# Optimization experiments

Hardware: AMD Instinct MI355X
Metric: run time of the kernel (lower is better)

The kernel has to match this reference:

```python
import jax, jax.numpy as jnp
import numpy as np

B, S, HID = 2, 2048, 2048
NH, NKV, D = 32, 4, 64
N_REP = NH // NKV
EPS = 1e-6
ROPE_THETA = 10000.0


def _rotate_half(x):
    h = x.shape[-1] // 2
    return jnp.concatenate([-x[..., h:], x[..., :h]], axis=-1)


def _rmsnorm(x, gamma):
    # RMSNorm over last dim (head_dim)
    return x * jax.lax.rsqrt(jnp.mean(x * x, axis=-1, keepdims=True) + EPS) * gamma


def setup_inputs() -> dict:
    key = jax.random.key(0)
    ks = jax.random.split(key, 8)
    hidden_states = jax.random.normal(ks[0], (B, S, HID), dtype=jnp.float32)
    # rotary cos/sin tables, shape [B, S, D]
    pos = jnp.arange(S, dtype=jnp.float32)
    inv_freq = 1.0 / (ROPE_THETA ** (jnp.arange(0, D, 2, dtype=jnp.float32) / D))
    freqs = pos[:, None] * inv_freq[None, :]            # [S, D/2]
    emb = jnp.concatenate([freqs, freqs], axis=-1)      # [S, D]
    cos = jnp.broadcast_to(jnp.cos(emb)[None], (B, S, D))
    sin = jnp.broadcast_to(jnp.sin(emb)[None], (B, S, D))
    sc = 0.02
    Wq = jax.random.normal(ks[1], (NH * D, HID), dtype=jnp.float32) * sc
    Wk = jax.random.normal(ks[2], (NKV * D, HID), dtype=jnp.float32) * sc
    Wv = jax.random.normal(ks[3], (NKV * D, HID), dtype=jnp.float32) * sc
    Wg = jax.random.normal(ks[4], (NH * D, HID), dtype=jnp.float32) * sc
    Wo = jax.random.normal(ks[5], (HID, NH * D), dtype=jnp.float32) * sc
    q_gamma = jnp.ones((D,), dtype=jnp.float32)
    k_gamma = jnp.ones((D,), dtype=jnp.float32)
    return dict(hidden_states=hidden_states, cos=cos, sin=sin,
                Wq=Wq, Wk=Wk, Wv=Wv, Wg=Wg, Wo=Wo,
                q_gamma=q_gamma, k_gamma=k_gamma)


def reference(hidden_states, cos, sin, Wq, Wk, Wv, Wg, Wo, q_gamma, k_gamma):
    b, s, _ = hidden_states.shape
    q = (hidden_states @ Wq.T).reshape(b, s, NH, D)
    k = (hidden_states @ Wk.T).reshape(b, s, NKV, D)
    v = (hidden_states @ Wv.T).reshape(b, s, NKV, D)
    gate = hidden_states @ Wg.T                       # [B, S, NH*D]
    # per-head RMSNorm on q/k
    q = _rmsnorm(q, q_gamma)
    k = _rmsnorm(k, k_gamma)
    # [B, H, S, D]
    q = q.transpose(0, 2, 1, 3)
    k = k.transpose(0, 2, 1, 3)
    v = v.transpose(0, 2, 1, 3)
    # RoPE (unsqueeze_dim=1)
    c = cos[:, None, :, :]
    sn = sin[:, None, :, :]
    q = q * c + _rotate_half(q) * sn
    k = k * c + _rotate_half(k) * sn
    # GQA: repeat kv heads
    kr = jnp.repeat(k, N_REP, axis=1)
    vr = jnp.repeat(v, N_REP, axis=1)
    scaling = D ** -0.5
    scores = jnp.einsum('bhqd,bhkd->bhqk', q, kr) * scaling
    w = jax.nn.softmax(scores.astype(jnp.float32), axis=-1).astype(q.dtype)
    out = jnp.einsum('bhqk,bhkd->bhqd', w, vr)
    out = out.transpose(0, 2, 1, 3).reshape(b, s, NH * D)
    out = out * jax.nn.sigmoid(gate)
    return out @ Wo.T
```

## Files before the change

kernel.cpp:

```cpp
#include <hip/hip_runtime.h>


#define LOG2E 1.44269504088896340736f

typedef __attribute__((ext_vector_type(4))) float f32x4;
typedef __attribute__((ext_vector_type(8))) short bf16x8;

__device__ __forceinline__ float bf2f(unsigned short u) {
  union { unsigned u; float f; } x; x.u = ((unsigned)u) << 16; return x.f;
}
__device__ __forceinline__ unsigned short f2bf(float f) {
  union { float f; unsigned u; } x; x.f = f;
  unsigned r = x.u + 0x7fffu + ((x.u >> 16) & 1u);
  return (unsigned short)(r >> 16);
}

__device__ __forceinline__ void async16(void* lds, const void* g) {
  __builtin_amdgcn_global_load_lds(
      (const __attribute__((address_space(1))) unsigned*)g,
      (__attribute__((address_space(3))) unsigned*)lds, 16, 0, 0);
}
__device__ __forceinline__ void lds_fence() {
  __asm__ volatile("s_waitcnt lgkmcnt(0)" ::: "memory");
}

__global__ __launch_bounds__(256) void cvt_all(
    const float* __restrict__ s0, const float* __restrict__ s1,
    const float* __restrict__ s2, const float* __restrict__ s3,
    const float* __restrict__ s4, const float* __restrict__ s5,
    unsigned short* __restrict__ d0, unsigned short* __restrict__ d1,
    unsigned short* __restrict__ d2, unsigned short* __restrict__ d3,
    unsigned short* __restrict__ d4, unsigned short* __restrict__ d5) {
  long i = (long)blockIdx.x * 256 + threadIdx.x;
  const float* s; unsigned short* d; long off;
  if      (i < 2097152) { s = s0; d = d0; off = 0; }
  else if (i < 3145728) { s = s1; d = d1; off = 2097152; }
  else if (i < 3276800) { s = s2; d = d2; off = 3145728; }
  else if (i < 3407872) { s = s3; d = d3; off = 3276800; }
  else if (i < 4456448) { s = s4; d = d4; off = 3407872; }
  else                  { s = s5; d = d5; off = 4456448; }
  long j = i - off;
  float4 v = reinterpret_cast<const float4*>(s)[j];
  ushort4 u;
  u.x = f2bf(v.x); u.y = f2bf(v.y); u.z = f2bf(v.z); u.w = f2bf(v.w);
  reinterpret_cast<ushort4*>(d)[j] = u;
}

__device__ __forceinline__ void gemm_main(
    const unsigned short* __restrict__ A, const unsigned short* __restrict__ W,
    int m0, int n0, int K, unsigned short* As, unsigned short* Bs,
    f32x4 acc[4][4]) {
  const int tid = threadIdx.x;
  const int w = tid >> 6, l = tid & 63, quad = l >> 4, l16 = l & 15;
  const int wm = (w & 1) * 64, wn = (w >> 1) * 64;

  const f32x4 Z4 = {0.f, 0.f, 0.f, 0.f};
#pragma unroll
  for (int i = 0; i < 4; i++)
#pragma unroll
    for (int j = 0; j < 4; j++) acc[i][j] = Z4;

  const int srow = tid >> 2;
  const int scol = (((tid & 3) ^ ((tid >> 3) & 3))) * 8;
  const unsigned short* gA = A + (size_t)(m0 + srow) * K + scol;
  const unsigned short* gB = W + (size_t)(n0 + srow) * K + scol;
  unsigned short* lA = As + tid * 8;
  unsigned short* lB = Bs + tid * 8;
  const int fsw = (quad ^ ((l16 >> 1) & 3)) * 8;

  for (int kb = 0; kb < K; kb += 32) {
    async16(lA,        gA + kb);
    async16(lA + 2048, gA + (size_t)64 * K + kb);
    async16(lB,        gB + kb);
    async16(lB + 2048, gB + (size_t)64 * K + kb);
    __syncthreads();

    bf16x8 af[4], bf[4];
#pragma unroll
    for (int mt = 0; mt < 4; mt++)
      af[mt] = *(const bf16x8*)&As[(wm + mt * 16 + l16) * 32 + fsw];
#pragma unroll
    for (int nt = 0; nt < 4; nt++)
      bf[nt] = *(const bf16x8*)&Bs[(wn + nt * 16 + l16) * 32 + fsw];
#pragma unroll
    for (int mt = 0; mt < 4; mt++)
#pragma unroll
      for (int nt = 0; nt < 4; nt++)
        acc[mt][nt] = __builtin_amdgcn_mfma_f32_16x16x32_bf16(
            af[mt], bf[nt], acc[mt][nt], 0, 0, 0);
    __syncthreads();
  }
}

__global__ __launch_bounds__(256) void gemm_qkvg(
    const unsigned short* __restrict__ X,
    const unsigned short* __restrict__ Wq, const unsigned short* __restrict__ Wk,
    const unsigned short* __restrict__ Wv, const unsigned short* __restrict__ Wg,
    const float* __restrict__ cosb, const float* __restrict__ sinb,
    const float* __restrict__ qg, const float* __restrict__ kg,
    unsigned short* __restrict__ Qn, unsigned short* __restrict__ Kn,
    unsigned short* __restrict__ Vt, unsigned short* __restrict__ gate) {
  __shared__ __attribute__((aligned(16))) unsigned short As[128 * 32];
  __shared__ __attribute__((aligned(16))) unsigned short Bs[128 * 32];
  const int ny = blockIdx.y;
  const unsigned short* W; int n0, type;
  if (ny < 16)      { W = Wq; n0 = ny * 128;        type = 0; }
  else if (ny < 18) { W = Wk; n0 = (ny - 16) * 128; type = 1; }
  else if (ny < 20) { W = Wv; n0 = (ny - 18) * 128; type = 2; }
  else              { W = Wg; n0 = (ny - 20) * 128; type = 3; }
  const int m0 = blockIdx.x * 128;

  f32x4 acc[4][4];
  gemm_main(X, W, m0, n0, 2048, As, Bs, acc);

  const int tid = threadIdx.x;
  const int w = tid >> 6, l = tid & 63, quad = l >> 4, l16 = l & 15;
  const int wm = (w & 1) * 64, wn = (w >> 1) * 64;

  if (type == 3) {
#pragma unroll
    for (int mt = 0; mt < 4; mt++)
#pragma unroll
      for (int r = 0; r < 4; r++) {
        int row = m0 + wm + mt * 16 + quad * 4 + r;
#pragma unroll
        for (int nt = 0; nt < 4; nt++)
          gate[(size_t)row * 2048 + n0 + wn + nt * 16 + l16] =
              f2bf(acc[mt][nt][r]);
      }
    return;
  }
  if (type == 2) {
#pragma unroll
    for (int mt = 0; mt < 4; mt++)
#pragma unroll
      for (int r = 0; r < 4; r++) {
        int row = m0 + wm + mt * 16 + quad * 4 + r;
        int b = row >> 11, s = row & 2047;
#pragma unroll
        for (int nt = 0; nt < 4; nt++) {
          int col = n0 + wn + nt * 16 + l16;
          int kvh = col >> 6, d = col & 63;
          Vt[((size_t)(b * 4 + kvh) * 64 + d) * 2048 + s] =
              f2bf(acc[mt][nt][r]);
        }
      }
    return;
  }

  const float* gamma = (type == 0) ? qg : kg;
  const float scale  = (type == 0) ? 0.125f : LOG2E;
  const int hb = (n0 + wn) >> 6;
  float gv[4];
#pragma unroll
  for (int nt = 0; nt < 4; nt++) gv[nt] = gamma[nt * 16 + l16];

#pragma unroll
  for (int mt = 0; mt < 4; mt++)
#pragma unroll
    for (int r = 0; r < 4; r++) {
      int row = m0 + wm + mt * 16 + quad * 4 + r;
      float ss = 0.f;
#pragma unroll
      for (int nt = 0; nt < 4; nt++) {
        float v = acc[mt][nt][r]; ss += v * v;
      }
#pragma unroll
      for (int off = 1; off < 16; off <<= 1) ss += __shfl_xor(ss, off);
      float rr = rsqrtf(ss * (1.0f / 64.0f) + 1e-6f);
      float xn[4];
#pragma unroll
      for (int nt = 0; nt < 4; nt++) xn[nt] = acc[mt][nt][r] * rr * gv[nt];
      int b = row >> 11, s = row & 2047;
      unsigned short* dst = (type == 0)
          ? Qn + ((size_t)(b * 32 + hb) * 2048 + s) * 64
          : Kn + ((size_t)(b * 4 + hb) * 2048 + s) * 64;
#pragma unroll
      for (int nt = 0; nt < 4; nt++) {
        int d = nt * 16 + l16;
        float rot = (nt < 2) ? -xn[nt ^ 2] : xn[nt ^ 2];
        float cv = cosb[(size_t)row * 64 + d];
        float sv = sinb[(size_t)row * 64 + d];
        dst[d] = f2bf((xn[nt] * cv + rot * sv) * scale);
      }
    }
}

__global__ __launch_bounds__(256) void gemm_out_k(
    const unsigned short* __restrict__ A, const unsigned short* __restrict__ W,
    float* __restrict__ C) {
  __shared__ __attribute__((aligned(16))) unsigned short As[128 * 32];
  __shared__ __attribute__((aligned(16))) unsigned short Bs[128 * 32];
  const int m0 = blockIdx.x * 128, n0 = blockIdx.y * 128;
  f32x4 acc[4][4];
  gemm_main(A, W, m0, n0, 2048, As, Bs, acc);
  const int tid = threadIdx.x;
  const int w = tid >> 6, l = tid & 63, quad = l >> 4, l16 = l & 15;
  const int wm = (w & 1) * 64, wn = (w >> 1) * 64;
#pragma unroll
  for (int mt = 0; mt < 4; mt++)
#pragma unroll
    for (int nt = 0; nt < 4; nt++) {
      int row = m0 + wm + mt * 16 + quad * 4;
      int col = n0 + wn + nt * 16 + l16;
#pragma unroll
      for (int r = 0; r < 4; r++)
        C[(size_t)(row + r) * 2048 + col] = acc[mt][nt][r];
    }
}

__global__ __launch_bounds__(256, 4) void attn(
    const unsigned short* __restrict__ Qn, const unsigned short* __restrict__ Kn,
    const unsigned short* __restrict__ Vt, const unsigned short* __restrict__ gate,
    unsigned short* __restrict__ act) {
  __shared__ __attribute__((aligned(16))) unsigned short smem[20480];
  unsigned short* Ps = smem + 16384;

  const int tid = threadIdx.x, w = tid >> 6, l = tid & 63;
  const int quad = l >> 4, l16 = l & 15, l7 = l16 & 7;
  const int bh = blockIdx.y, b = bh >> 5, h = bh & 31, kvh = h >> 3;
  const int q0 = blockIdx.x * 128;

  const unsigned short* Qg = Qn + ((size_t)(b * 32 + h) * 2048 + q0) * 64;
  const unsigned short* Kg = Kn + (size_t)(b * 4 + kvh) * 2048 * 64;
  const unsigned short* Vg = Vt + (size_t)(b * 4 + kvh) * 64 * 2048;
  unsigned short* Pw = Ps + w * 1024;

  const int kq_src = ((tid & 7) ^ ((tid >> 3) & 7)) * 8;

#pragma unroll
  for (int i = 0; i < 4; i++)
    async16(smem + i * 2048 + tid * 8,
            Qg + (size_t)(i * 32 + (tid >> 3)) * 64 + kq_src);
  __syncthreads();
  bf16x8 qf[2][2];
#pragma unroll
  for (int mt = 0; mt < 2; mt++)
#pragma unroll
    for (int ks = 0; ks < 2; ks++) {
      int row = w * 32 + mt * 16 + l16;
      qf[mt][ks] = *(const bf16x8*)&smem[row * 64 + ((ks * 4 + quad) ^ l7) * 8];
    }
  __syncthreads();

  const f32x4 Z4 = {0.f, 0.f, 0.f, 0.f};
  f32x4 O[2][4];
  float lp[2][4];
#pragma unroll
  for (int mt = 0; mt < 2; mt++) {
#pragma unroll
    for (int nt = 0; nt < 4; nt++) O[mt][nt] = Z4;
#pragma unroll
    for (int r = 0; r < 4; r++) lp[mt][r] = 0.f;
  }

#pragma unroll
  for (int i = 0; i < 2; i++) {
    async16(smem + i * 2048 + tid * 8,
            Kg + (size_t)(i * 32 + (tid >> 3)) * 64 + kq_src);
    async16(smem + 4096 + i * 2048 + tid * 8,
            Vg + (size_t)(i * 32 + (tid >> 3)) * 2048 + kq_src);
  }

  for (int kt = 0; kt < 32; kt++) {
    __syncthreads();

    if (kt < 31) {
      unsigned short* nb = smem + ((kt + 1) & 1) * 8192;
      const int s1 = (kt + 1) * 64;
#pragma unroll
      for (int i = 0; i < 2; i++) {
        async16(nb + i * 2048 + tid * 8,
                Kg + (size_t)(s1 + i * 32 + (tid >> 3)) * 64 + kq_src);
        async16(nb + 4096 + i * 2048 + tid * 8,
                Vg + (size_t)(i * 32 + (tid >> 3)) * 2048 + s1 + kq_src);
      }
    }

    unsigned short* Ks  = smem + (kt & 1) * 8192;
    unsigned short* Vts = Ks + 4096;

    f32x4 sc[2][4];
#pragma unroll
    for (int mt = 0; mt < 2; mt++)
#pragma unroll
      for (int nt = 0; nt < 4; nt++) sc[mt][nt] = Z4;
#pragma unroll
    for (int nt = 0; nt < 4; nt++) {
      int row = nt * 16 + l16;
      bf16x8 kf0 = *(const bf16x8*)&Ks[row * 64 + (quad ^ l7) * 8];
      bf16x8 kf1 = *(const bf16x8*)&Ks[row * 64 + ((4 + quad) ^ l7) * 8];
#pragma unroll
      for (int mt = 0; mt < 2; mt++) {
        sc[mt][nt] = __builtin_amdgcn_mfma_f32_16x16x32_bf16(qf[mt][0], kf0, sc[mt][nt], 0, 0, 0);
        sc[mt][nt] = __builtin_amdgcn_mfma_f32_16x16x32_bf16(qf[mt][1], kf1, sc[mt][nt], 0, 0, 0);
      }
    }

#pragma unroll
    for (int ks2 = 0; ks2 < 2; ks2++) {
#pragma unroll
      for (int mt = 0; mt < 2; mt++)
#pragma unroll
        for (int ntl = 0; ntl < 2; ntl++) {
          int nt = ks2 * 2 + ntl;
#pragma unroll
          for (int r = 0; r < 4; r++) {
            float p = __builtin_amdgcn_exp2f(sc[mt][nt][r]);
            union { float f; unsigned u; } x; x.f = p;
            union { unsigned u; float f; } t; t.u = x.u & 0xffff0000u;
            lp[mt][r] += t.f;
            int q = mt * 16 + quad * 4 + r;
            int c = ntl * 2 + (l16 >> 3);
            int phys = c ^ ((q >> 1) & 3);
            Pw[q * 32 + phys * 8 + l7] = (unsigned short)(x.u >> 16);
          }
        }
      lds_fence();

      bf16x8 pf[2];
#pragma unroll
      for (int mt = 0; mt < 2; mt++) {
        int q = mt * 16 + l16;
        int phys = quad ^ ((l16 >> 1) & 3);
        pf[mt] = *(const bf16x8*)&Pw[q * 32 + phys * 8];
      }
#pragma unroll
      for (int nt2 = 0; nt2 < 4; nt2++) {
        int d = nt2 * 16 + l16;
        bf16x8 vf = *(const bf16x8*)&Vts[d * 64 + ((ks2 * 4 + quad) ^ l7) * 8];
#pragma unroll
        for (int mt = 0; mt < 2; mt++)
          O[mt][nt2] = __builtin_amdgcn_mfma_f32_16x16x32_bf16(
              pf[mt], vf, O[mt][nt2], 0, 0, 0);
      }
      lds_fence();
    }
  }

#pragma unroll
  for (int mt = 0; mt < 2; mt++)
#pragma unroll
    for (int r = 0; r < 4; r++) {
      float s = lp[mt][r];
#pragma unroll
      for (int off = 1; off < 16; off <<= 1) s += __shfl_xor(s, off);
      lp[mt][r] = s;
    }

#pragma unroll
  for (int mt = 0; mt < 2; mt++) {
    float inv[4];
#pragma unroll
    for (int r = 0; r < 4; r++) inv[r] = 1.0f / lp[mt][r];
#pragma unroll
    for (int nt = 0; nt < 4; nt++)
#pragma unroll
      for (int r = 0; r < 4; r++) {
        int srow = q0 + w * 32 + mt * 16 + quad * 4 + r;
        int col = h * 64 + nt * 16 + l16;
        size_t off = (size_t)(b * 2048 + srow) * 2048 + col;
        float g = bf2f(gate[off]);
        float sig = 1.0f / (1.0f + __builtin_amdgcn_exp2f(-g * LOG2E));
        act[off] = f2bf(O[mt][nt][r] * inv[r] * sig);
      }
  }
}

extern "C" void kernel_launch(void* const* d_in, const int* in_sizes, int n_in,
                              void* d_out, int out_size, void* d_ws, size_t ws_size,
                              hipStream_t stream) {
  const float* hid  = (const float*)d_in[0];
  const float* cosb = (const float*)d_in[1];
  const float* sinb = (const float*)d_in[2];
  const float* Wq   = (const float*)d_in[3];
  const float* Wk   = (const float*)d_in[4];
  const float* Wv   = (const float*)d_in[5];
  const float* Wg   = (const float*)d_in[6];
  const float* Wo   = (const float*)d_in[7];
  const float* qg   = (const float*)d_in[8];
  const float* kg   = (const float*)d_in[9];
  float* out = (float*)d_out;

  char* ws = (char*)d_ws;
  unsigned short* Xb   = (unsigned short*)(ws);
  unsigned short* WqB  = (unsigned short*)(ws + 16777216);
  unsigned short* WkB  = (unsigned short*)(ws + 25165824);
  unsigned short* WvB  = (unsigned short*)(ws + 26214400);
  unsigned short* WgB  = (unsigned short*)(ws + 27262976);
  unsigned short* WoB  = (unsigned short*)(ws + 35651584);
  unsigned short* gate = (unsigned short*)(ws + 44040192);
  unsigned short* Qn   = (unsigned short*)(ws + 60817408);
  unsigned short* Kn   = (unsigned short*)(ws + 77594624);
  unsigned short* Vt   = (unsigned short*)(ws + 79691776);
  unsigned short* act = WqB;

  cvt_all<<<dim3(21504), dim3(256), 0, stream>>>(
      hid, Wq, Wk, Wv, Wg, Wo, Xb, WqB, WkB, WvB, WgB, WoB);

  gemm_qkvg<<<dim3(32, 36), dim3(256), 0, stream>>>(
      Xb, WqB, WkB, WvB, WgB, cosb, sinb, qg, kg, Qn, Kn, Vt, gate);

  attn<<<dim3(16, 64), dim3(256), 0, stream>>>(Qn, Kn, Vt, gate, act);

  gemm_out_k<<<dim3(32, 16), dim3(256), 0, stream>>>(act, WoB, out);
}
```

Measured before the change: 395.9 us.

## Pipeline GEMMs with multi-buffered async LDS loads and 128x256 tiles

Replaces the single-buffered 128x128 GEMM main loop with a 128x256 tile run by 512 threads. A is double-buffered and B triple-buffered in LDS, with async global-to-LDS prefetch of the next K-step overlapping the MFMA work. K-steps grow to 64 with an 8-way XOR swizzle, plus explicit barriers, waitcnt and setprio scheduling. The QKVG and output GEMM grids are halved to match. This aims to hide global-load latency and raise reuse per block, at the cost of 128KB of LDS per block, fewer blocks, and fragile hand-tuned synchronisation.

```diff
diff --git a/kernel.cpp b/kernel.cpp
--- a/kernel.cpp
+++ b/kernel.cpp
@@ -46,13 +46,14 @@
   reinterpret_cast<ushort4*>(d)[j] = u;
 }
 
-__device__ __forceinline__ void gemm_main(
+__device__ __forceinline__ void gemm_main_big(
     const unsigned short* __restrict__ A, const unsigned short* __restrict__ W,
-    int m0, int n0, int K, unsigned short* As, unsigned short* Bs,
-    f32x4 acc[4][4]) {
+    int m0, int n0, unsigned short* lds, f32x4 acc[4][4]) {
   const int tid = threadIdx.x;
   const int w = tid >> 6, l = tid & 63, quad = l >> 4, l16 = l & 15;
+  const int l7 = l16 & 7;
   const int wm = (w & 1) * 64, wn = (w >> 1) * 64;
+  const int rlo = tid >> 3, ch = tid & 7;
 
   const f32x4 Z4 = {0.f, 0.f, 0.f, 0.f};
 #pragma unroll
@@ -60,39 +61,102 @@
 #pragma unroll
     for (int j = 0; j < 4; j++) acc[i][j] = Z4;
 
-  const int srow = tid >> 2;
-  const int scol = (((tid & 3) ^ ((tid >> 3) & 3))) * 8;
-  const unsigned short* gA = A + (size_t)(m0 + srow) * K + scol;
-  const unsigned short* gB = W + (size_t)(n0 + srow) * K + scol;
-  unsigned short* lA = As + tid * 8;
-  unsigned short* lB = Bs + tid * 8;
-  const int fsw = (quad ^ ((l16 >> 1) & 3)) * 8;
-
-  for (int kb = 0; kb < K; kb += 32) {
-    async16(lA,        gA + kb);
-    async16(lA + 2048, gA + (size_t)64 * K + kb);
-    async16(lB,        gB + kb);
-    async16(lB + 2048, gB + (size_t)64 * K + kb);
-    __syncthreads();
-
-    bf16x8 af[4], bf[4];
-#pragma unroll
-    for (int mt = 0; mt < 4; mt++)
-      af[mt] = *(const bf16x8*)&As[(wm + mt * 16 + l16) * 32 + fsw];
+  const unsigned short* gA = A + (size_t)(m0 + rlo) * 2048 + ((ch ^ (rlo & 7)) * 8);
+  const unsigned short* gB = W + (size_t)(n0 + rlo) * 2048 + ((ch ^ (rlo & 7)) * 8);
+
+  int arow[4], brow[4];
+#pragma unroll
+  for (int mt = 0; mt < 4; mt++) arow[mt] = (wm + mt * 16 + l16) * 64;
+#pragma unroll
+  for (int nt = 0; nt < 4; nt++) brow[nt] = (wn + nt * 16 + l16) * 64;
+  const int x0 = (quad ^ l7) * 8;
+  const int x1 = ((4 + quad) ^ l7) * 8;
+
+  unsigned short* const bA = lds;
+  unsigned short* const bB = lds + 16384;
+
+  async16(bA + tid * 8,          gA);
+  async16(bA + 4096 + tid * 8,   gA + 131072);
+  async16(bB + tid * 8,          gB);
+  async16(bB + 4096 + tid * 8,   gB + 131072);
+  async16(bB + 8192 + tid * 8,   gB + 262144);
+  async16(bB + 12288 + tid * 8,  gB + 393216);
+  async16(bB + 16384 + tid * 8,  gB + 64);
+  async16(bB + 20480 + tid * 8,  gB + 131072 + 64);
+  async16(bB + 24576 + tid * 8,  gB + 262144 + 64);
+  async16(bB + 28672 + tid * 8,  gB + 393216 + 64);
+  __asm__ volatile("s_waitcnt vmcnt(4)" ::: "memory");
+  __builtin_amdgcn_s_barrier();
+
+  int cb = 0;
+  for (int t = 0; t < 32; ++t) {
+    unsigned short* cbA = bA + (t & 1) * 8192;
+    unsigned short* cbB = bB + cb * 16384;
+
+    if (t < 31) {
+      unsigned short* nA = bA + ((t + 1) & 1) * 8192;
+      const int ko = (t + 1) * 64;
+      async16(nA + tid * 8,        gA + ko);
+      async16(nA + 4096 + tid * 8, gA + 131072 + ko);
+    }
+    bf16x8 a0[4], b0[4];
+#pragma unroll
+    for (int mt = 0; mt < 4; mt++)
+      a0[mt] = *(const bf16x8*)&cbA[arow[mt] + x0];
 #pragma unroll
     for (int nt = 0; nt < 4; nt++)
-      bf[nt] = *(const bf16x8*)&Bs[(wn + nt * 16 + l16) * 32 + fsw];
+      b0[nt] = *(const bf16x8*)&cbB[brow[nt] + x0];
+    __builtin_amdgcn_s_barrier();
+    __asm__ volatile("s_waitcnt lgkmcnt(0)" ::: "memory");
+    __builtin_amdgcn_sched_barrier(0);
+    __builtin_amdgcn_s_setprio(1);
 #pragma unroll
     for (int mt = 0; mt < 4; mt++)
 #pragma unroll
       for (int nt = 0; nt < 4; nt++)
         acc[mt][nt] = __builtin_amdgcn_mfma_f32_16x16x32_bf16(
-            af[mt], bf[nt], acc[mt][nt], 0, 0, 0);
-    __syncthreads();
-  }
-}
-
-__global__ __launch_bounds__(256) void gemm_qkvg(
+            a0[mt], b0[nt], acc[mt][nt], 0, 0, 0);
+    __builtin_amdgcn_s_setprio(0);
+    __builtin_amdgcn_s_barrier();
+
+    if (t < 30) {
+      int nb = cb + 2; if (nb >= 3) nb -= 3;
+      unsigned short* nB = bB + nb * 16384;
+      const int ko = (t + 2) * 64;
+      async16(nB + tid * 8,         gB + ko);
+      async16(nB + 4096 + tid * 8,  gB + 131072 + ko);
+      async16(nB + 8192 + tid * 8,  gB + 262144 + ko);
+      async16(nB + 12288 + tid * 8, gB + 393216 + ko);
+    }
+    bf16x8 a1[4], b1[4];
+#pragma unroll
+    for (int mt = 0; mt < 4; mt++)
+      a1[mt] = *(const bf16x8*)&cbA[arow[mt] + x1];
+#pragma unroll
+    for (int nt = 0; nt < 4; nt++)
+      b1[nt] = *(const bf16x8*)&cbB[brow[nt] + x1];
+    __builtin_amdgcn_s_barrier();
+    __asm__ volatile("s_waitcnt lgkmcnt(0)" ::: "memory");
+    __builtin_amdgcn_sched_barrier(0);
+    __builtin_amdgcn_s_setprio(1);
+#pragma unroll
+    for (int mt = 0; mt < 4; mt++)
+#pragma unroll
+      for (int nt = 0; nt < 4; nt++)
+        acc[mt][nt] = __builtin_amdgcn_mfma_f32_16x16x32_bf16(
+            a1[mt], b1[nt], acc[mt][nt], 0, 0, 0);
+    __builtin_amdgcn_s_setprio(0);
+    if (t < 30) {
+      __asm__ volatile("s_waitcnt vmcnt(4)" ::: "memory");
+    } else if (t == 30) {
+      __asm__ volatile("s_waitcnt vmcnt(0)" ::: "memory");
+    }
+    __builtin_amdgcn_s_barrier();
+    cb++; if (cb == 3) cb = 0;
+  }
+}
+
+__global__ __launch_bounds__(512, 2) void gemm_qkvg(
     const unsigned short* __restrict__ X,
     const unsigned short* __restrict__ Wq, const unsigned short* __restrict__ Wk,
     const unsigned short* __restrict__ Wv, const unsigned short* __restrict__ Wg,
@@ -100,18 +164,17 @@
     const float* __restrict__ qg, const float* __restrict__ kg,
     unsigned short* __restrict__ Qn, unsigned short* __restrict__ Kn,
     unsigned short* __restrict__ Vt, unsigned short* __restrict__ gate) {
-  __shared__ __attribute__((aligned(16))) unsigned short As[128 * 32];
-  __shared__ __attribute__((aligned(16))) unsigned short Bs[128 * 32];
+  __shared__ __attribute__((aligned(16))) unsigned short lds[65536];
   const int ny = blockIdx.y;
   const unsigned short* W; int n0, type;
-  if (ny < 16)      { W = Wq; n0 = ny * 128;        type = 0; }
-  else if (ny < 18) { W = Wk; n0 = (ny - 16) * 128; type = 1; }
-  else if (ny < 20) { W = Wv; n0 = (ny - 18) * 128; type = 2; }
-  else              { W = Wg; n0 = (ny - 20) * 128; type = 3; }
+  if (ny < 8)       { W = Wq; n0 = ny * 256;        type = 0; }
+  else if (ny == 8) { W = Wk; n0 = 0;               type = 1; }
+  else if (ny == 9) { W = Wv; n0 = 0;               type = 2; }
+  else              { W = Wg; n0 = (ny - 10) * 256; type = 3; }
   const int m0 = blockIdx.x * 128;
 
   f32x4 acc[4][4];
-  gemm_main(X, W, m0, n0, 2048, As, Bs, acc);
+  gemm_main_big(X, W, m0, n0, lds, acc);
 
   const int tid = threadIdx.x;
   const int w = tid >> 6, l = tid & 63, quad = l >> 4, l16 = l & 15;
@@ -139,7 +202,7 @@
         int b = row >> 11, s = row & 2047;
 #pragma unroll
         for (int nt = 0; nt < 4; nt++) {
-          int col = n0 + wn + nt * 16 + l16;
+          int col = wn + nt * 16 + l16;
           int kvh = col >> 6, d = col & 63;
           Vt[((size_t)(b * 4 + kvh) * 64 + d) * 2048 + s] =
               f2bf(acc[mt][nt][r]);
@@ -186,14 +249,13 @@
     }
 }
 
-__global__ __launch_bounds__(256) void gemm_out_k(
+__global__ __launch_bounds__(512, 2) void gemm_out_k(
     const unsigned short* __restrict__ A, const unsigned short* __restrict__ W,
     float* __restrict__ C) {
-  __shared__ __attribute__((aligned(16))) unsigned short As[128 * 32];
-  __shared__ __attribute__((aligned(16))) unsigned short Bs[128 * 32];
-  const int m0 = blockIdx.x * 128, n0 = blockIdx.y * 128;
+  __shared__ __attribute__((aligned(16))) unsigned short lds[65536];
+  const int m0 = blockIdx.x * 128, n0 = blockIdx.y * 256;
   f32x4 acc[4][4];
-  gemm_main(A, W, m0, n0, 2048, As, Bs, acc);
+  gemm_main_big(A, W, m0, n0, lds, acc);
   const int tid = threadIdx.x;
   const int w = tid >> 6, l = tid & 63, quad = l >> 4, l16 = l & 15;
   const int wm = (w & 1) * 64, wn = (w >> 1) * 64;
@@ -398,10 +460,10 @@
   cvt_all<<<dim3(21504), dim3(256), 0, stream>>>(
       hid, Wq, Wk, Wv, Wg, Wo, Xb, WqB, WkB, WvB, WgB, WoB);
 
-  gemm_qkvg<<<dim3(32, 36), dim3(256), 0, stream>>>(
+  gemm_qkvg<<<dim3(32, 18), dim3(512), 0, stream>>>(
       Xb, WqB, WkB, WvB, WgB, cosb, sinb, qg, kg, Qn, Kn, Vt, gate);
 
   attn<<<dim3(16, 64), dim3(256), 0, stream>>>(Qn, Kn, Vt, gate, act);
 
-  gemm_out_k<<<dim3(32, 16), dim3(256), 0, stream>>>(act, WoB, out);
-}
+  gemm_out_k<<<dim3(32, 8), dim3(512), 0, stream>>>(act, WoB, out);
+}
```

Measured after the change: 366.1 us. 1.08x faster.
